# Kernel tuning notes

Measured on AMD Instinct MI355X. Metric: run time of the kernel, lower is better.

Reference implementation:

```python
import jax, jax.numpy as jnp
import numpy as np

N_NODES = 100000
N_EDGES = 1600000
IN_DIM, HID_DIM, OUT_DIM = 128, 64, 40


def gcn_conv(x, src, dst, deg_inv_sqrt, W, b):
    # PyG GCNConv: out[dst] += norm(e) * (x @ W)[src] ; norm = d^-1/2[src]*d^-1/2[dst]
    h = x @ W                                   # [N, out]
    norm = deg_inv_sqrt[src] * deg_inv_sqrt[dst]  # [E]
    msgs = h[src] * norm[:, None]               # [E, out] gather
    out = jax.ops.segment_sum(msgs, dst, num_segments=x.shape[0])  # scatter-add
    return out + b


def setup_inputs() -> dict:
    key = jax.random.key(0)
    k1, k2, k3, k4, k5, k6 = jax.random.split(key, 6)
    x = jax.random.normal(k1, (N_NODES, IN_DIM), dtype=jnp.float32)
    edge_index = jax.random.randint(k2, (2, N_EDGES), 0, N_NODES, dtype=jnp.int64)
    # Glorot-style init for linear weights, zero bias (as in GCNConv defaults)
    W1 = jax.random.normal(k3, (IN_DIM, HID_DIM), dtype=jnp.float32) / np.sqrt(IN_DIM)
    b1 = jnp.zeros((HID_DIM,), dtype=jnp.float32)
    W2 = jax.random.normal(k4, (HID_DIM, OUT_DIM), dtype=jnp.float32) / np.sqrt(HID_DIM)
    b2 = jnp.zeros((OUT_DIM,), dtype=jnp.float32)
    return {"x": x, "edge_index": edge_index, "W1": W1, "b1": b1, "W2": W2, "b2": b2}


def reference(x, edge_index, W1, b1, W2, b2):
    N = x.shape[0]
    loop = jnp.arange(N, dtype=edge_index.dtype)
    src = jnp.concatenate([edge_index[0], loop])  # add self-loops
    dst = jnp.concatenate([edge_index[1], loop])
    # symmetric normalization: degree over destination (col) with unit edge weights
    deg = jax.ops.segment_sum(jnp.ones_like(dst, dtype=x.dtype), dst, num_segments=N)
    deg_inv_sqrt = jnp.where(deg > 0, jax.lax.rsqrt(deg), 0.0)

    h = jax.nn.relu(gcn_conv(x, src, dst, deg_inv_sqrt, W1, b1))
    h = gcn_conv(h, src, dst, deg_inv_sqrt, W2, b2)
    return jax.nn.log_softmax(h, axis=1)
```

## Files before the change

kernel.cpp:

```cpp
#include <hip/hip_runtime.h>
#include <hip/hip_bf16.h>
#include <math.h>

typedef long long i64;

__device__ __forceinline__ float bfu(unsigned short u) {
    union { unsigned int i; float f; } v; v.i = ((unsigned)u) << 16; return v.f;
}
__device__ __forceinline__ unsigned short f2b(float f) {
    __hip_bfloat16 h = __float2bfloat16(f);
    return *reinterpret_cast<unsigned short*>(&h);
}

#define NPB_SHIFT 9
#define NPB 512
#define LCAP 16384
#define P1C 4096

__global__ void k_zeroB(int* __restrict__ bcnt, int B) {
    int t = threadIdx.x;
    if (t <= B) bcnt[t] = 0;
}

__global__ __launch_bounds__(256) void k_p1count(
    const int* __restrict__ dst, int E, int B, int* __restrict__ bcnt) {
    __shared__ int lb[256];
    int t = threadIdx.x;
    lb[t] = 0; __syncthreads();
    int cpb = (E + gridDim.x - 1) / gridDim.x;
    int s0 = blockIdx.x * cpb, s1 = min(E, s0 + cpb);
    for (int i = s0 + t; i < s1; i += 256)
        atomicAdd(&lb[dst[i] >> NPB_SHIFT], 1);
    __syncthreads();
    if (t < B && lb[t]) atomicAdd(&bcnt[t], lb[t]);
}

__global__ void k_scanB(const int* __restrict__ bcnt, int B, int E,
                        int* __restrict__ bstart, int* __restrict__ cursor) {
    __shared__ int s[256];
    int t = threadIdx.x;
    int v = (t < B) ? bcnt[t] : 0;
    s[t] = v; __syncthreads();
    for (int off = 1; off < 256; off <<= 1) {
        int u = (t >= off) ? s[t - off] : 0;
        __syncthreads();
        s[t] += u;
        __syncthreads();
    }
    int excl = s[t] - v;
    if (t < B) { bstart[t] = excl; cursor[t] = excl; }
    if (t == 0) bstart[B] = E;
}

__global__ __launch_bounds__(256) void k_p1place(
    const int* __restrict__ src, const int* __restrict__ dst, int E, int B,
    int* __restrict__ cursor, uint2* __restrict__ pairs) {
    __shared__ int ls_s[P1C];
    __shared__ int ls_d[P1C];
    __shared__ int lb[256];
    __shared__ int lbase[256];
    int t = threadIdx.x;
    int s0 = blockIdx.x * P1C, s1 = min(E, s0 + P1C), n = s1 - s0;
    lb[t] = 0; __syncthreads();
    for (int i = t; i < n; i += 256) {
        int d = dst[s0 + i];
        ls_d[i] = d;
        ls_s[i] = src[s0 + i];
        atomicAdd(&lb[d >> NPB_SHIFT], 1);
    }
    __syncthreads();
    if (t < B && lb[t]) lbase[t] = atomicAdd(&cursor[t], lb[t]);
    __syncthreads();
    lb[t] = 0; __syncthreads();
    for (int i = t; i < n; i += 256) {
        int d = ls_d[i];
        int bkt = d >> NPB_SHIFT;
        int slot = atomicAdd(&lb[bkt], 1);
        pairs[lbase[bkt] + slot] = make_uint2((unsigned)ls_s[i], (unsigned)d);
    }
}

__global__ __launch_bounds__(512) void k_p2(
    const uint2* __restrict__ pairs, const int* __restrict__ bstart,
    int* __restrict__ rowptr, float* __restrict__ dinv,
    int* __restrict__ col, int N, int E) {
    __shared__ int lcnt[NPB];
    __shared__ int lscan[NPB];
    __shared__ int lcol[LCAP];
    int b = blockIdx.x, t = threadIdx.x;
    int lo = b << NPB_SHIFT, hi = min(N, lo + NPB), nn = hi - lo;
    int e0 = bstart[b], e1 = bstart[b + 1];
    lcnt[t] = 0; __syncthreads();
    for (int i = e0 + t; i < e1; i += 512)
        atomicAdd(&lcnt[(int)pairs[i].y - lo], 1);
    __syncthreads();
    int myc = (t < nn) ? lcnt[t] : 0;
    lscan[t] = myc; __syncthreads();
    for (int off = 1; off < 512; off <<= 1) {
        int u = (t >= off) ? lscan[t - off] : 0;
        __syncthreads();
        lscan[t] += u;
        __syncthreads();
    }
    if (t < nn) {
        rowptr[lo + t] = e0 + lscan[t] - myc;
        dinv[lo + t] = rsqrtf((float)(myc + 1));
    }
    if (t == 0 && hi == N) rowptr[N] = E;
    __syncthreads();
    lscan[t] -= myc;
    lcnt[t] = 0;
    __syncthreads();
    for (int i = e0 + t; i < e1; i += 512) {
        uint2 p = pairs[i];
        int n = (int)p.y - lo;
        int slot = atomicAdd(&lcnt[n], 1);
        int idx = lscan[n] + slot;
        if (idx < LCAP) lcol[idx] = (int)p.x;
    }
    __syncthreads();
    int cnt = e1 - e0;
    for (int i = t; i < cnt; i += 512) col[e0 + i] = lcol[i];
}


template<int D, int F, int THREADS, int RPB>
__global__ __launch_bounds__(THREADS) void k_gemm(
    const float* __restrict__ X, const float* __restrict__ W,
    const float* __restrict__ dinv, unsigned short* __restrict__ out, int N) {
    constexpr int CG = F / 4;
    constexpr int XLD = D + 4;
    __shared__ float Ws[D * F];
    __shared__ float Xs[RPB * XLD];
    int tid = threadIdx.x;
    int row0 = blockIdx.x * RPB;

    for (int i = tid; i < D * F / 4; i += THREADS)
        ((float4*)Ws)[i] = ((const float4*)W)[i];
    for (int i = tid; i < RPB * D / 4; i += THREADS) {
        int r = i / (D / 4), kk = i % (D / 4);
        int grow = row0 + r;
        float4 v = make_float4(0.f, 0.f, 0.f, 0.f);
        if (grow < N) v = *(const float4*)&X[(size_t)grow * D + kk * 4];
        *(float4*)&Xs[r * XLD + kk * 4] = v;
    }
    __syncthreads();

    int cg = tid % CG, rg = tid / CG;
    float acc[4][4] = {};
    const float* xb = &Xs[(rg * 4) * XLD];
    #pragma unroll 4
    for (int k = 0; k < D; ++k) {
        float4 w = *(float4*)&Ws[k * F + cg * 4];
        float x0 = xb[0 * XLD + k];
        float x1 = xb[1 * XLD + k];
        float x2 = xb[2 * XLD + k];
        float x3 = xb[3 * XLD + k];
        acc[0][0] += x0 * w.x; acc[0][1] += x0 * w.y; acc[0][2] += x0 * w.z; acc[0][3] += x0 * w.w;
        acc[1][0] += x1 * w.x; acc[1][1] += x1 * w.y; acc[1][2] += x1 * w.z; acc[1][3] += x1 * w.w;
        acc[2][0] += x2 * w.x; acc[2][1] += x2 * w.y; acc[2][2] += x2 * w.z; acc[2][3] += x2 * w.w;
        acc[3][0] += x3 * w.x; acc[3][1] += x3 * w.y; acc[3][2] += x3 * w.z; acc[3][3] += x3 * w.w;
    }
    #pragma unroll
    for (int i = 0; i < 4; i++) {
        int grow = row0 + rg * 4 + i;
        if (grow < N) {
            float dv = dinv[grow];
            ushort4 o;
            o.x = f2b(acc[i][0] * dv);
            o.y = f2b(acc[i][1] * dv);
            o.z = f2b(acc[i][2] * dv);
            o.w = f2b(acc[i][3] * dv);
            *(ushort4*)&out[(size_t)grow * F + cg * 4] = o;
        }
    }
}


template<bool L1>
__global__ __launch_bounds__(256) void k_agg(
    const unsigned short* __restrict__ gsrc, const int* __restrict__ rowptr,
    const int* __restrict__ col, const float* __restrict__ dinv,
    const float* __restrict__ b1, unsigned short* __restrict__ gout, int N) {
    int gw = (int)((blockIdx.x * 256u + threadIdx.x) >> 6);
    int lane = threadIdx.x & 63;
    int li = lane & 31;
    int node = gw * 2 + (lane >> 5);
    bool valid = node < N;
    int r0 = 0, r1 = 0;
    if (valid) { r0 = rowptr[node]; r1 = rowptr[node + 1]; }
    size_t fo = (size_t)(li * 2);
    float s0 = 0.f, s1 = 0.f;
    if (valid) {
        ushort2 u = *(const ushort2*)(gsrc + (((size_t)node) << 6) + fo);
        s0 = bfu(u.x); s1 = bfu(u.y);
    }
    int e = r0;
    for (; e + 16 <= r1; e += 16) {
        int cc[16];
        #pragma unroll
        for (int j = 0; j < 16; j++) cc[j] = col[e + j];
        float va[16], vb[16];
        #pragma unroll
        for (int j = 0; j < 16; j++) {
            ushort2 u = *(const ushort2*)(gsrc + (((size_t)cc[j]) << 6) + fo);
            va[j] = bfu(u.x); vb[j] = bfu(u.y);
        }
        #pragma unroll
        for (int s = 1; s < 16; s <<= 1)
            #pragma unroll
            for (int j = 0; j < 16; j += 2 * s) { va[j] += va[j + s]; vb[j] += vb[j + s]; }
        s0 += va[0]; s1 += vb[0];
    }
    for (; e + 4 <= r1; e += 4) {
        int c0 = col[e], c1 = col[e + 1], c2 = col[e + 2], c3 = col[e + 3];
        ushort2 u0 = *(const ushort2*)(gsrc + (((size_t)c0) << 6) + fo);
        ushort2 u1 = *(const ushort2*)(gsrc + (((size_t)c1) << 6) + fo);
        ushort2 u2 = *(const ushort2*)(gsrc + (((size_t)c2) << 6) + fo);
        ushort2 u3 = *(const ushort2*)(gsrc + (((size_t)c3) << 6) + fo);
        s0 += (bfu(u0.x) + bfu(u1.x)) + (bfu(u2.x) + bfu(u3.x));
        s1 += (bfu(u0.y) + bfu(u1.y)) + (bfu(u2.y) + bfu(u3.y));
    }
    for (; e < r1; ++e) {
        ushort2 u = *(const ushort2*)(gsrc + (((size_t)col[e]) << 6) + fo);
        s0 += bfu(u.x); s1 += bfu(u.y);
    }
    if (valid) {
        float dv = dinv[node];
        float o0, o1;
        if (L1) {
            o0 = dv * fmaxf(dv * s0 + b1[li * 2 + 0], 0.f);
            o1 = dv * fmaxf(dv * s1 + b1[li * 2 + 1], 0.f);
        } else {
            o0 = dv * s0;
            o1 = dv * s1;
        }
        ushort2 w;
        w.x = f2b(o0); w.y = f2b(o1);
        *(ushort2*)(gout + (((size_t)node) << 6) + fo) = w;
    }
}


__global__ __launch_bounds__(256) void k_gemm2s(
    const unsigned short* __restrict__ t, const float* __restrict__ W2,
    const float* __restrict__ b2, float* __restrict__ out, int N) {
    __shared__ unsigned short Xs[256 * 72];
    __shared__ float W2s[64 * 40];
    __shared__ float b2s[40];
    int tid = threadIdx.x;
    int row0 = blockIdx.x * 256;
    for (int i = tid; i < 640; i += 256)
        ((float4*)W2s)[i] = ((const float4*)W2)[i];
    if (tid < 40) b2s[tid] = b2[tid];
    for (int c = tid; c < 2048; c += 256) {
        int r = c >> 3, j = c & 7;
        int gr = row0 + r;
        uint4 v = make_uint4(0u, 0u, 0u, 0u);
        if (gr < N) v = *(const uint4*)(t + (((size_t)gr) << 6) + j * 8);
        *(uint4*)(Xs + r * 72 + j * 8) = v;
    }
    __syncthreads();
    int row = row0 + tid;
    if (row >= N) return;
    float acc[40];
    #pragma unroll
    for (int c = 0; c < 40; c++) acc[c] = b2s[c];
    const unsigned short* xr = Xs + tid * 72;
    for (int k = 0; k < 64; k++) {
        float x = bfu(xr[k]);
        #pragma unroll
        for (int j = 0; j < 10; j++) {
            float4 w = ((const float4*)(W2s + k * 40))[j];
            acc[4 * j + 0] += x * w.x;
            acc[4 * j + 1] += x * w.y;
            acc[4 * j + 2] += x * w.z;
            acc[4 * j + 3] += x * w.w;
        }
    }
    float m = acc[0];
    #pragma unroll
    for (int c = 1; c < 40; c++) m = fmaxf(m, acc[c]);
    float p = 0.f;
    #pragma unroll
    for (int c = 0; c < 40; c++) p += __expf(acc[c] - m);
    float l = __logf(p) + m;
    float* orow = out + (size_t)row * 40;
    #pragma unroll
    for (int j = 0; j < 10; j++) {
        float4 ov;
        ov.x = acc[4 * j + 0] - l;
        ov.y = acc[4 * j + 1] - l;
        ov.z = acc[4 * j + 2] - l;
        ov.w = acc[4 * j + 3] - l;
        *(float4*)(orow + 4 * j) = ov;
    }
}


extern "C" void kernel_launch(void* const* d_in, const int* in_sizes, int n_in,
                              void* d_out, int out_size, void* d_ws, size_t ws_size,
                              hipStream_t stream) {
    const float* x  = (const float*)d_in[0];
    const int*   ei = (const int*)d_in[1];
    const float* W1 = (const float*)d_in[2];
    const float* b1 = (const float*)d_in[3];
    const float* W2 = (const float*)d_in[4];
    const float* b2 = (const float*)d_in[5];
    float* out = (float*)d_out;

    const int N = in_sizes[0] / 128;
    const int E = in_sizes[1] / 2;
    const int B = (N + NPB - 1) >> NPB_SHIFT;
    const int* src = ei;
    const int* dst = ei + E;

    char* w = (char*)d_ws;
    size_t off = 0;
    auto alloc = [&](size_t bytes) -> char* {
        char* p = w + off;
        off += (bytes + 255) & ~(size_t)255;
        return p;
    };
    int*   bcnt   = (int*)alloc((size_t)(B + 1) * 4);
    int*   bstart = (int*)alloc((size_t)(B + 1) * 4);
    int*   cursor = (int*)alloc((size_t)B * 4);
    int*   rowptr = (int*)alloc((size_t)(N + 1) * 4);
    float* dinv   = (float*)alloc((size_t)N * 4);
    int*   col    = (int*)alloc((size_t)E * 4 + 256);
    size_t shbytes = (size_t)E * 8 > (size_t)N * 64 * 2 ? (size_t)E * 8 : (size_t)N * 64 * 2;
    char*  sh     = alloc(shbytes);
    unsigned short* q = (unsigned short*)alloc((size_t)N * 64 * 2);
    uint2* pairs  = (uint2*)sh;
    unsigned short* g1 = (unsigned short*)sh;
    unsigned short* t  = (unsigned short*)sh;

    k_zeroB<<<1, 256, 0, stream>>>(bcnt, B);
    k_p1count<<<256, 256, 0, stream>>>(dst, E, B, bcnt);
    k_scanB<<<1, 256, 0, stream>>>(bcnt, B, E, bstart, cursor);
    int nch = (E + P1C - 1) / P1C;
    k_p1place<<<nch, 256, 0, stream>>>(src, dst, E, B, cursor, pairs);
    k_p2<<<B, 512, 0, stream>>>(pairs, bstart, rowptr, dinv, col, N, E);

    int nwaves = (N + 1) / 2;
    int aggblocks = (nwaves + 3) / 4;

    k_gemm<128, 64, 256, 64><<<(N + 63) / 64, 256, 0, stream>>>(x, W1, dinv, g1, N);
    k_agg<true><<<aggblocks, 256, 0, stream>>>(g1, rowptr, col, dinv, b1, q, N);

    k_agg<false><<<aggblocks, 256, 0, stream>>>(q, rowptr, col, dinv, b1, t, N);
    k_gemm2s<<<(N + 255) / 256, 256, 0, stream>>>(t, W2, b2, out, N);
}
```

Before: 193.0 us.

## Use bf16 MFMA for the first-layer GEMM with swizzled LDS tiles

Replaces the FP32 scalar-FMA first GEMM (X·W1) with a matrix-core kernel that converts X and W1 to bf16 in shared memory, using XOR-swizzled layouts to avoid bank conflicts, and runs 16x16x32 bf16 MFMA instructions, 128 rows per block. The aim is to cut the compute cost of the dense projection. The trade-off is lower input precision, since X and W are rounded to bf16 before the multiply, and output stores become 2-byte scattered writes. The renaming in the aggregation kernel is cosmetic.

```diff
diff --git a/kernel.cpp b/kernel.cpp
--- a/kernel.cpp
+++ b/kernel.cpp
@@ -3,6 +3,8 @@
 #include <math.h>
 
 typedef long long i64;
+typedef __attribute__((ext_vector_type(8))) short short8v;
+typedef __attribute__((ext_vector_type(4))) float f32x4;
 
 __device__ __forceinline__ float bfu(unsigned short u) {
     union { unsigned int i; float f; } v; v.i = ((unsigned)u) << 16; return v.f;
@@ -124,56 +126,83 @@
 }
 
 
-template<int D, int F, int THREADS, int RPB>
-__global__ __launch_bounds__(THREADS) void k_gemm(
+__global__ __launch_bounds__(256) void k_gemm1m(
     const float* __restrict__ X, const float* __restrict__ W,
     const float* __restrict__ dinv, unsigned short* __restrict__ out, int N) {
-    constexpr int CG = F / 4;
-    constexpr int XLD = D + 4;
-    __shared__ float Ws[D * F];
-    __shared__ float Xs[RPB * XLD];
+    __shared__ unsigned short Xs[128 * 128];
+    __shared__ unsigned short Wt[64 * 128];
     int tid = threadIdx.x;
-    int row0 = blockIdx.x * RPB;
-
-    for (int i = tid; i < D * F / 4; i += THREADS)
-        ((float4*)Ws)[i] = ((const float4*)W)[i];
-    for (int i = tid; i < RPB * D / 4; i += THREADS) {
-        int r = i / (D / 4), kk = i % (D / 4);
-        int grow = row0 + r;
+    int row0 = blockIdx.x << 7;
+
+    for (int i = tid; i < 2048; i += 256) {
+        float4 v = *(const float4*)(W + i * 4);
+        int k = (i * 4) >> 6, n = (i * 4) & 63;
+        int kb = k * 2;
+        *(unsigned short*)((char*)Wt + (n + 0) * 256 + (kb ^ (((n + 0) & 7) << 4))) = f2b(v.x);
+        *(unsigned short*)((char*)Wt + (n + 1) * 256 + (kb ^ (((n + 1) & 7) << 4))) = f2b(v.y);
+        *(unsigned short*)((char*)Wt + (n + 2) * 256 + (kb ^ (((n + 2) & 7) << 4))) = f2b(v.z);
+        *(unsigned short*)((char*)Wt + (n + 3) * 256 + (kb ^ (((n + 3) & 7) << 4))) = f2b(v.w);
+    }
+    for (int i = tid; i < 4096; i += 256) {
+        int r = i >> 5, c4 = i & 31;
+        int gr = row0 + r;
         float4 v = make_float4(0.f, 0.f, 0.f, 0.f);
-        if (grow < N) v = *(const float4*)&X[(size_t)grow * D + kk * 4];
-        *(float4*)&Xs[r * XLD + kk * 4] = v;
-    }
-    __syncthreads();
-
-    int cg = tid % CG, rg = tid / CG;
-    float acc[4][4] = {};
-    const float* xb = &Xs[(rg * 4) * XLD];
-    #pragma unroll 4
-    for (int k = 0; k < D; ++k) {
-        float4 w = *(float4*)&Ws[k * F + cg * 4];
-        float x0 = xb[0 * XLD + k];
-        float x1 = xb[1 * XLD + k];
-        float x2 = xb[2 * XLD + k];
-        float x3 = xb[3 * XLD + k];
-        acc[0][0] += x0 * w.x; acc[0][1] += x0 * w.y; acc[0][2] += x0 * w.z; acc[0][3] += x0 * w.w;
-        acc[1][0] += x1 * w.x; acc[1][1] += x1 * w.y; acc[1][2] += x1 * w.z; acc[1][3] += x1 * w.w;
-        acc[2][0] += x2 * w.x; acc[2][1] += x2 * w.y; acc[2][2] += x2 * w.z; acc[2][3] += x2 * w.w;
-        acc[3][0] += x3 * w.x; acc[3][1] += x3 * w.y; acc[3][2] += x3 * w.z; acc[3][3] += x3 * w.w;
-    }
-    #pragma unroll
-    for (int i = 0; i < 4; i++) {
-        int grow = row0 + rg * 4 + i;
-        if (grow < N) {
-            float dv = dinv[grow];
-            ushort4 o;
-            o.x = f2b(acc[i][0] * dv);
-            o.y = f2b(acc[i][1] * dv);
-            o.z = f2b(acc[i][2] * dv);
-            o.w = f2b(acc[i][3] * dv);
-            *(ushort4*)&out[(size_t)grow * F + cg * 4] = o;
+        if (gr < N) v = *(const float4*)(X + (size_t)gr * 128 + c4 * 4);
+        ushort4 h;
+        h.x = f2b(v.x); h.y = f2b(v.y); h.z = f2b(v.z); h.w = f2b(v.w);
+        *(ushort4*)((char*)Xs + r * 256 + ((c4 * 8) ^ ((r & 7) << 4))) = h;
+    }
+    __syncthreads();
+
+    int wid = tid >> 6, lane = tid & 63;
+    int l15 = lane & 15, lg = lane >> 4;
+    int wrow = wid * 32;
+
+    f32x4 acc[2][4];
+    #pragma unroll
+    for (int fr = 0; fr < 2; fr++)
+        #pragma unroll
+        for (int fc = 0; fc < 4; fc++) acc[fr][fc] = (f32x4){0.f, 0.f, 0.f, 0.f};
+
+    #pragma unroll
+    for (int ks = 0; ks < 4; ks++) {
+        int kbyte = ks * 64 + lg * 16;
+        int ra0 = wrow + l15, ra1 = wrow + 16 + l15;
+        short8v a0 = *(short8v*)((char*)Xs + ra0 * 256 + (kbyte ^ ((ra0 & 7) << 4)));
+        short8v a1 = *(short8v*)((char*)Xs + ra1 * 256 + (kbyte ^ ((ra1 & 7) << 4)));
+        int swb = kbyte ^ ((l15 & 7) << 4);
+        short8v b0 = *(short8v*)((char*)Wt + (l15) * 256 + swb);
+        short8v b1 = *(short8v*)((char*)Wt + (16 + l15) * 256 + swb);
+        short8v b2 = *(short8v*)((char*)Wt + (32 + l15) * 256 + swb);
+        short8v b3 = *(short8v*)((char*)Wt + (48 + l15) * 256 + swb);
+        acc[0][0] = __builtin_amdgcn_mfma_f32_16x16x32_bf16(a0, b0, acc[0][0], 0, 0, 0);
+        acc[0][1] = __builtin_amdgcn_mfma_f32_16x16x32_bf16(a0, b1, acc[0][1], 0, 0, 0);
+        acc[0][2] = __builtin_amdgcn_mfma_f32_16x16x32_bf16(a0, b2, acc[0][2], 0, 0, 0);
+        acc[0][3] = __builtin_amdgcn_mfma_f32_16x16x32_bf16(a0, b3, acc[0][3], 0, 0, 0);
+        acc[1][0] = __builtin_amdgcn_mfma_f32_16x16x32_bf16(a1, b0, acc[1][0], 0, 0, 0);
+        acc[1][1] = __builtin_amdgcn_mfma_f32_16x16x32_bf16(a1, b1, acc[1][1], 0, 0, 0);
+        acc[1][2] = __builtin_amdgcn_mfma_f32_16x16x32_bf16(a1, b2, acc[1][2], 0, 0, 0);
+        acc[1][3] = __builtin_amdgcn_mfma_f32_16x16x32_bf16(a1, b3, acc[1][3], 0, 0, 0);
+    }
+
+    float dv[2][4];
+    #pragma unroll
+    for (int fr = 0; fr < 2; fr++)
+        #pragma unroll
+        for (int reg = 0; reg < 4; reg++) {
+            int grow = row0 + wrow + fr * 16 + lg * 4 + reg;
+            dv[fr][reg] = (grow < N) ? dinv[grow] : 0.f;
         }
-    }
+    #pragma unroll
+    for (int fr = 0; fr < 2; fr++)
+        #pragma unroll
+        for (int fc = 0; fc < 4; fc++)
+            #pragma unroll
+            for (int reg = 0; reg < 4; reg++) {
+                int grow = row0 + wrow + fr * 16 + lg * 4 + reg;
+                if (grow < N)
+                    out[(size_t)grow * 64 + fc * 16 + l15] = f2b(acc[fr][fc][reg] * dv[fr][reg]);
+            }
 }
 
 
@@ -226,14 +255,14 @@
         s0 += bfu(u.x); s1 += bfu(u.y);
     }
     if (valid) {
-        float dv = dinv[node];
+        float dvn = dinv[node];
         float o0, o1;
         if (L1) {
-            o0 = dv * fmaxf(dv * s0 + b1[li * 2 + 0], 0.f);
-            o1 = dv * fmaxf(dv * s1 + b1[li * 2 + 1], 0.f);
+            o0 = dvn * fmaxf(dvn * s0 + b1[li * 2 + 0], 0.f);
+            o1 = dvn * fmaxf(dvn * s1 + b1[li * 2 + 1], 0.f);
         } else {
-            o0 = dv * s0;
-            o1 = dv * s1;
+            o0 = dvn * s0;
+            o1 = dvn * s1;
         }
         ushort2 w;
         w.x = f2b(o0); w.y = f2b(o1);
@@ -345,7 +374,7 @@
     int nwaves = (N + 1) / 2;
     int aggblocks = (nwaves + 3) / 4;
 
-    k_gemm<128, 64, 256, 64><<<(N + 63) / 64, 256, 0, stream>>>(x, W1, dinv, g1, N);
+    k_gemm1m<<<(N + 127) / 128, 256, 0, stream>>>(x, W1, dinv, g1, N);
     k_agg<true><<<aggblocks, 256, 0, stream>>>(g1, rowptr, col, dinv, b1, q, N);
 
     k_agg<false><<<aggblocks, 256, 0, stream>>>(q, rowptr, col, dinv, b1, t, N);
```

Result: faster. 181.7 us (-5.8%).
